# Optimization experiments

Measured on AMD Instinct MI355X. Metric: run time of the kernel, lower is better.

The kernel has to match this reference:

```python
import jax, jax.numpy as jnp
import numpy as np

VEC, HID, B, S = 1280, 128, 4, 256
EPS = 1e-5


def _ln(x):
    m = x.mean(-1, keepdims=True)
    v = ((x - m) ** 2).mean(-1, keepdims=True)
    return (x - m) / jnp.sqrt(v + EPS)


def _add_attn(q_in, kv_in, Wq, Wk, wv):
    # Additive (Bahdanau) attention: scores[b,i,j] = wv . tanh(q[b,i] + k[b,j])
    q = q_in @ Wq            # [B, Sq, H]
    k = kv_in @ Wk           # [B, Sk, H]
    feat = jnp.tanh(q[:, :, None, :] + k[:, None, :, :])   # [B, Sq, Sk, H]
    scores = jnp.einsum('bijh,h->bij', feat, wv)
    attn = jax.nn.softmax(scores, axis=-1)
    return jnp.einsum('bij,bjd->bid', attn, kv_in)          # values = kv_in


def _res_fc(x, W1, b1, W2, b2):
    return jnp.maximum(x @ W1 + b1, 0.0) @ W2 + b2 + x


def setup_inputs() -> dict:
    key = jax.random.key(0)
    ks = iter(jax.random.split(key, 64))
    d = {
        'X': jax.random.normal(next(ks), (B, S, VEC), dtype=jnp.float32),
        'lys_pos': 100,
    }
    sc = 0.02
    for i in (1, 2, 3, 4):
        d[f'Wq{i}'] = jax.random.normal(next(ks), (VEC, HID), dtype=jnp.float32) * sc
        d[f'Wk{i}'] = jax.random.normal(next(ks), (VEC, HID), dtype=jnp.float32) * sc
        d[f'wv{i}'] = jax.random.normal(next(ks), (HID,), dtype=jnp.float32) * sc
    for i in (1, 2, 3):
        d[f'rW1_{i}'] = jax.random.normal(next(ks), (VEC, HID), dtype=jnp.float32) * sc
        d[f'rb1_{i}'] = jnp.zeros((HID,), dtype=jnp.float32)
        d[f'rW2_{i}'] = jax.random.normal(next(ks), (HID, VEC), dtype=jnp.float32) * sc
        d[f'rb2_{i}'] = jnp.zeros((VEC,), dtype=jnp.float32)
    d['hW1'] = jax.random.normal(next(ks), (VEC, 32), dtype=jnp.float32) * sc
    d['hb1'] = jnp.zeros((32,), dtype=jnp.float32)
    d['hW2'] = jax.random.normal(next(ks), (32, 12), dtype=jnp.float32) * sc
    d['hb2'] = jnp.zeros((12,), dtype=jnp.float32)
    d['hW3'] = jax.random.normal(next(ks), (12, 2), dtype=jnp.float32) * sc
    d['hb3'] = jnp.zeros((2,), dtype=jnp.float32)
    return d


def reference(X, lys_pos,
              Wq1, Wk1, wv1, Wq2, Wk2, wv2, Wq3, Wk3, wv3, Wq4, Wk4, wv4,
              rW1_1, rb1_1, rW2_1, rb2_1,
              rW1_2, rb1_2, rW2_2, rb2_2,
              rW1_3, rb1_3, rW2_3, rb2_3,
              hW1, hb1, hW2, hb2, hW3, hb3):
    X = X.astype(jnp.float32)
    X = _ln(_add_attn(X, X, Wq1, Wk1, wv1) + X)
    X = _res_fc(X, rW1_1, rb1_1, rW2_1, rb2_1)
    X = _ln(_add_attn(X, X, Wq2, Wk2, wv2) + X)
    X = _res_fc(X, rW1_2, rb1_2, rW2_2, rb2_2)
    X = _ln(_add_attn(X, X, Wq3, Wk3, wv3) + X)
    X = _res_fc(X, rW1_3, rb1_3, rW2_3, rb2_3)
    X_lys = X[:, lys_pos, :][:, None, :]                    # [B, 1, VEC]
    X_lys = _ln(_add_attn(X_lys, X, Wq4, Wk4, wv4) + X_lys)
    h = jnp.maximum(X_lys @ hW1 + hb1, 0.0)                 # dropout = identity (eval)
    h = jnp.maximum(h @ hW2 + hb2, 0.0)
    logits = (h @ hW3 + hb3)[:, 0, :]                       # squeeze(1) -> [B, 2]
    return logits
```

## Files before the change

### kernel.cpp

```cpp
#include <hip/hip_runtime.h>


#define DEV __device__ __forceinline__

static constexpr int VEC = 1280;
static constexpr int HID = 128;
static constexpr int BB  = 4;
static constexpr int SS  = 256;
static constexpr int MROWS = BB * SS;

DEV float ftanh(float x) {
  float e = __expf(2.0f * x);
  return 1.0f - __fdividef(2.0f, e + 1.0f);
}

DEV float waveSum(float v) {
#pragma unroll
  for (int off = 32; off > 0; off >>= 1) v += __shfl_xor(v, off, 64);
  return v;
}
DEV float waveMax(float v) {
#pragma unroll
  for (int off = 32; off > 0; off >>= 1) v = fmaxf(v, __shfl_xor(v, off, 64));
  return v;
}
DEV float blockSum(float v, float* red) {
  v = waveSum(v);
  int tid = threadIdx.x;
  if ((tid & 63) == 0) red[tid >> 6] = v;
  __syncthreads();
  float r = (red[0] + red[1]) + (red[2] + red[3]);
  __syncthreads();
  return r;
}
DEV float blockMax(float v, float* red) {
  v = waveMax(v);
  int tid = threadIdx.x;
  if ((tid & 63) == 0) red[tid >> 6] = v;
  __syncthreads();
  float r = fmaxf(fmaxf(red[0], red[1]), fmaxf(red[2], red[3]));
  __syncthreads();
  return r;
}

template <int ZMODE, bool ABRELU, bool OBIAS, bool ORES>
__global__ __launch_bounds__(256) void gemm_k(
    const float* __restrict__ A, long sAb,
    const float* __restrict__ B0, const float* __restrict__ B1, int nSplitB,
    long sBb, int ldB,
    float* __restrict__ C, long sCb,
    const float* __restrict__ aBias, const float* __restrict__ oBias,
    const float* __restrict__ res,
    int N, int K, int kChunk) {
  const int n0 = blockIdx.x * 64;
  const int m0 = blockIdx.y * 64;
  const int z  = blockIdx.z;

  const float* Ab = A + (ZMODE == 0 ? (long)z * sAb : 0L);
  float*       Cb = C + (ZMODE == 0 ? (long)z * sCb : 0L);
  const float* Bsel;
  int nb;
  if (n0 < nSplitB) { Bsel = B0; nb = n0; } else { Bsel = B1; nb = n0 - nSplitB; }
  Bsel += (ZMODE == 0 ? (long)z * sBb : 0L);

  const int kBeg = (ZMODE == 1) ? z * kChunk : 0;
  const int kEnd = (ZMODE == 1) ? kBeg + kChunk : K;

  __shared__ float As[16][68];
  __shared__ float Bs[16][68];

  const int tid = threadIdx.x;
  const int tx = tid & 15, ty = tid >> 4;
  const int ar = tid >> 2, ac = (tid & 3) << 2;
  const int br = tid >> 4, bc = (tid & 15) << 2;

  float acc[4][4] = {};

  for (int kt = kBeg; kt < kEnd; kt += 16) {
    float4 a4 = *(const float4*)(Ab + (size_t)(m0 + ar) * K + kt + ac);
    float4 b4 = *(const float4*)(Bsel + (size_t)(kt + br) * ldB + nb + bc);
    if (ABRELU) {
      float4 bz = *(const float4*)(aBias + kt + ac);
      a4.x = fmaxf(a4.x + bz.x, 0.0f);
      a4.y = fmaxf(a4.y + bz.y, 0.0f);
      a4.z = fmaxf(a4.z + bz.z, 0.0f);
      a4.w = fmaxf(a4.w + bz.w, 0.0f);
    }
    __syncthreads();
    As[ac + 0][ar] = a4.x;
    As[ac + 1][ar] = a4.y;
    As[ac + 2][ar] = a4.z;
    As[ac + 3][ar] = a4.w;
    *(float4*)&Bs[br][bc] = b4;
    __syncthreads();
#pragma unroll
    for (int kk = 0; kk < 16; ++kk) {
      const float4 av = *(const float4*)&As[kk][ty << 2];
      const float4 bv = *(const float4*)&Bs[kk][tx << 2];
      const float a[4] = {av.x, av.y, av.z, av.w};
      const float b[4] = {bv.x, bv.y, bv.z, bv.w};
#pragma unroll
      for (int i = 0; i < 4; ++i)
#pragma unroll
        for (int j = 0; j < 4; ++j) acc[i][j] = fmaf(a[i], b[j], acc[i][j]);
    }
  }

#pragma unroll
  for (int i = 0; i < 4; ++i) {
    const int m = m0 + (ty << 2) + i;
#pragma unroll
    for (int j = 0; j < 4; ++j) {
      const int n = n0 + (tx << 2) + j;
      float v = acc[i][j];
      if (ZMODE == 1) {
        atomicAdd(&Cb[(size_t)m * N + n], v);
      } else {
        if (OBIAS) v += oBias[n];
        if (ORES) v += res[(size_t)m * N + n];
        Cb[(size_t)m * N + n] = v;
      }
    }
  }
}

__global__ __launch_bounds__(256) void scores_k(const float* __restrict__ QK,
                                                const float* __restrict__ wv,
                                                float* __restrict__ attn) {
  const int i = blockIdx.x, b = blockIdx.y;
  const int tid = threadIdx.x;
  __shared__ float qs[128], wvs[128];
  __shared__ float red[4];
  if (tid < 128) {
    qs[tid] = QK[((size_t)(b * 256 + i)) * 256 + tid];
    wvs[tid] = wv[tid];
  }
  __syncthreads();
  const float* Kr = QK + ((size_t)(b * 256 + tid)) * 256 + 128;
  float s = 0.0f;
#pragma unroll 8
  for (int h = 0; h < 128; h += 4) {
    float4 k4 = *(const float4*)(Kr + h);
    s += wvs[h + 0] * ftanh(qs[h + 0] + k4.x);
    s += wvs[h + 1] * ftanh(qs[h + 1] + k4.y);
    s += wvs[h + 2] * ftanh(qs[h + 2] + k4.z);
    s += wvs[h + 3] * ftanh(qs[h + 3] + k4.w);
  }
  const float mx = blockMax(s, red);
  const float e = __expf(s - mx);
  const float tot = blockSum(e, red);
  attn[((size_t)(b * 256 + i)) * 256 + tid] = e / tot;
}

__global__ __launch_bounds__(256) void ln_k(const float* __restrict__ A,
                                            const float* __restrict__ Xin,
                                            float* __restrict__ Y) {
  __shared__ float red[4];
  const int r = blockIdx.x, tid = threadIdx.x;
  const float* a = A + (size_t)r * VEC;
  const float* x = Xin + (size_t)r * VEC;
  float v[5];
  float sum = 0.0f;
#pragma unroll
  for (int k = 0; k < 5; ++k) {
    const int d = tid + k * 256;
    v[k] = a[d] + x[d];
    sum += v[k];
  }
  sum = blockSum(sum, red);
  const float m = sum * (1.0f / VEC);
  float sq = 0.0f;
#pragma unroll
  for (int k = 0; k < 5; ++k) {
    const float dl = v[k] - m;
    sq += dl * dl;
  }
  sq = blockSum(sq, red);
  const float rstd = rsqrtf(sq * (1.0f / VEC) + 1e-5f);
  float* y = Y + (size_t)r * VEC;
#pragma unroll
  for (int k = 0; k < 5; ++k) y[tid + k * 256] = (v[k] - m) * rstd;
}

__global__ __launch_bounds__(256) void scores4_k(const float* __restrict__ QK,
                                                 const float* __restrict__ wv,
                                                 const int* __restrict__ lys,
                                                 float* __restrict__ attn4) {
  const int b = blockIdx.x, tid = threadIdx.x;
  __shared__ float qs[128], wvs[128];
  __shared__ float red[4];
  const int lp = lys[0];
  if (tid < 128) {
    qs[tid] = QK[((size_t)(b * 256 + lp)) * 256 + tid];
    wvs[tid] = wv[tid];
  }
  __syncthreads();
  const float* Kr = QK + ((size_t)(b * 256 + tid)) * 256 + 128;
  float s = 0.0f;
#pragma unroll 8
  for (int h = 0; h < 128; h += 4) {
    float4 k4 = *(const float4*)(Kr + h);
    s += wvs[h + 0] * ftanh(qs[h + 0] + k4.x);
    s += wvs[h + 1] * ftanh(qs[h + 1] + k4.y);
    s += wvs[h + 2] * ftanh(qs[h + 2] + k4.z);
    s += wvs[h + 3] * ftanh(qs[h + 3] + k4.w);
  }
  const float mx = blockMax(s, red);
  const float e = __expf(s - mx);
  const float tot = blockSum(e, red);
  attn4[b * 256 + tid] = e / tot;
}

__global__ __launch_bounds__(256) void attn4_out_ln_k(const float* __restrict__ attn4,
                                                      const float* __restrict__ X3,
                                                      const int* __restrict__ lys,
                                                      float* __restrict__ Xlys) {
  const int b = blockIdx.x, tid = threadIdx.x;
  __shared__ float aw[256];
  __shared__ float red[4];
  aw[tid] = attn4[b * 256 + tid];
  __syncthreads();
  float acc[5] = {0, 0, 0, 0, 0};
  const float* Xb = X3 + (size_t)b * SS * VEC;
  for (int j = 0; j < 256; ++j) {
    const float a = aw[j];
    const float* xr = Xb + (size_t)j * VEC;
#pragma unroll
    for (int k = 0; k < 5; ++k) acc[k] = fmaf(a, xr[tid + k * 256], acc[k]);
  }
  const int lp = lys[0];
  const float* xq = Xb + (size_t)lp * VEC;
  float sum = 0.0f;
#pragma unroll
  for (int k = 0; k < 5; ++k) {
    acc[k] += xq[tid + k * 256];
    sum += acc[k];
  }
  sum = blockSum(sum, red);
  const float m = sum * (1.0f / VEC);
  float sq = 0.0f;
#pragma unroll
  for (int k = 0; k < 5; ++k) {
    const float dl = acc[k] - m;
    sq += dl * dl;
  }
  sq = blockSum(sq, red);
  const float rstd = rsqrtf(sq * (1.0f / VEC) + 1e-5f);
#pragma unroll
  for (int k = 0; k < 5; ++k) Xlys[b * VEC + tid + k * 256] = (acc[k] - m) * rstd;
}

__global__ __launch_bounds__(256) void head_k(const float* __restrict__ Xlys,
                                              const float* __restrict__ hW1,
                                              const float* __restrict__ hb1,
                                              const float* __restrict__ hW2,
                                              const float* __restrict__ hb2,
                                              const float* __restrict__ hW3,
                                              const float* __restrict__ hb3,
                                              float* __restrict__ out) {
  const int b = blockIdx.x, tid = threadIdx.x;
  __shared__ float xr[1280];
  __shared__ float partial[256];
  __shared__ float h1s[32], h2s[12];
  for (int k = tid; k < 1280; k += 256) xr[k] = Xlys[b * VEC + k];
  __syncthreads();
  const int n = tid & 31, s = tid >> 5;
  float p = 0.0f;
  for (int k = s * 160; k < s * 160 + 160; ++k) p = fmaf(xr[k], hW1[k * 32 + n], p);
  partial[tid] = p;
  __syncthreads();
  if (tid < 32) {
    float v = 0.0f;
#pragma unroll
    for (int s2 = 0; s2 < 8; ++s2) v += partial[s2 * 32 + tid];
    h1s[tid] = fmaxf(v + hb1[tid], 0.0f);
  }
  __syncthreads();
  if (tid < 12) {
    float v = 0.0f;
#pragma unroll
    for (int k = 0; k < 32; ++k) v = fmaf(h1s[k], hW2[k * 12 + tid], v);
    h2s[tid] = fmaxf(v + hb2[tid], 0.0f);
  }
  __syncthreads();
  if (tid < 2) {
    float v = 0.0f;
#pragma unroll
    for (int k = 0; k < 12; ++k) v = fmaf(h2s[k], hW3[k * 2 + tid], v);
    out[b * 2 + tid] = v + hb3[tid];
  }
}

extern "C" void kernel_launch(void* const* d_in, const int* in_sizes, int n_in,
                              void* d_out, int out_size, void* d_ws, size_t ws_size,
                              hipStream_t stream) {
  const float* X = (const float*)d_in[0];
  const int* lys = (const int*)d_in[1];
  const float* Wq[4] = {(const float*)d_in[2], (const float*)d_in[5],
                        (const float*)d_in[8], (const float*)d_in[11]};
  const float* Wk[4] = {(const float*)d_in[3], (const float*)d_in[6],
                        (const float*)d_in[9], (const float*)d_in[12]};
  const float* wv[4] = {(const float*)d_in[4], (const float*)d_in[7],
                        (const float*)d_in[10], (const float*)d_in[13]};
  const float* rW1[3] = {(const float*)d_in[14], (const float*)d_in[18],
                         (const float*)d_in[22]};
  const float* rb1[3] = {(const float*)d_in[15], (const float*)d_in[19],
                         (const float*)d_in[23]};
  const float* rW2[3] = {(const float*)d_in[16], (const float*)d_in[20],
                         (const float*)d_in[24]};
  const float* rb2[3] = {(const float*)d_in[17], (const float*)d_in[21],
                         (const float*)d_in[25]};
  const float* hW1 = (const float*)d_in[26];
  const float* hb1 = (const float*)d_in[27];
  const float* hW2 = (const float*)d_in[28];
  const float* hb2 = (const float*)d_in[29];
  const float* hW3 = (const float*)d_in[30];
  const float* hb3 = (const float*)d_in[31];
  float* out = (float*)d_out;

  float* ws = (float*)d_ws;
  float* QK    = ws;
  float* attn  = QK + 262144;
  float* big0  = attn + 262144;
  float* big1  = big0 + 1310720;
  float* big2  = big1 + 1310720;
  float* Hacc  = big2 + 1310720;
  float* attn4 = Hacc + 131072;
  float* Xlys  = attn4 + 1024;

  float* bufA[3] = {big0, big1, big0};
  float* bufY[3] = {big1, big2, big2};
  float* bufO[3] = {big0, big1, big0};

  const int NSPLIT_NONE = 1 << 30;
  const float* Xin = X;

  for (int l = 0; l < 3; ++l) {
    hipMemsetAsync(QK, 0, (size_t)MROWS * 256 * sizeof(float), stream);
    gemm_k<1, false, false, false><<<dim3(4, 16, 4), 256, 0, stream>>>(
        Xin, 0, Wq[l], Wk[l], HID, 0, HID, QK, 0, nullptr, nullptr, nullptr,
        256, VEC, 320);
    scores_k<<<dim3(SS, BB), 256, 0, stream>>>(QK, wv[l], attn);
    gemm_k<0, false, false, false><<<dim3(20, 4, 4), 256, 0, stream>>>(
        attn, (long)SS * SS, Xin, Xin, NSPLIT_NONE, (long)SS * VEC, VEC,
        bufA[l], (long)SS * VEC, nullptr, nullptr, nullptr, VEC, SS, 0);
    ln_k<<<dim3(MROWS), 256, 0, stream>>>(bufA[l], Xin, bufY[l]);
    hipMemsetAsync(Hacc, 0, (size_t)MROWS * HID * sizeof(float), stream);
    gemm_k<1, false, false, false><<<dim3(2, 16, 8), 256, 0, stream>>>(
        bufY[l], 0, rW1[l], rW1[l], NSPLIT_NONE, 0, HID, Hacc, 0, nullptr,
        nullptr, nullptr, HID, VEC, 160);
    gemm_k<0, true, true, true><<<dim3(20, 16, 1), 256, 0, stream>>>(
        Hacc, 0, rW2[l], rW2[l], NSPLIT_NONE, 0, VEC, bufO[l], 0, rb1[l],
        rb2[l], bufY[l], VEC, HID, 0);
    Xin = bufO[l];
  }

  hipMemsetAsync(QK, 0, (size_t)MROWS * 256 * sizeof(float), stream);
  gemm_k<1, false, false, false><<<dim3(4, 16, 4), 256, 0, stream>>>(
      Xin, 0, Wq[3], Wk[3], HID, 0, HID, QK, 0, nullptr, nullptr, nullptr,
      256, VEC, 320);
  scores4_k<<<dim3(BB), 256, 0, stream>>>(QK, wv[3], lys, attn4);
  attn4_out_ln_k<<<dim3(BB), 256, 0, stream>>>(attn4, Xin, lys, Xlys);
  head_k<<<dim3(BB), 256, 0, stream>>>(Xlys, hW1, hb1, hW2, hb2, hW3, hb3, out);
}
```

Measured before the change: 529.3 us.

## Replace atomic split-K with partial buffers, batch score rows, fuse tail kernels

Split-K GEMMs now write per-chunk partial buffers instead of doing atomicAdd into memset-zeroed outputs, and consumers sum the four partials on load. This removes the memsets and the atomics. The scores kernel handles 8 query rows per block so each K row load is reused across them. The residual add moves into the attention-output GEMM epilogue, leaving a simpler LN. The last layer computes only the K projection plus a single-row Q projection, and the four tail kernels are fused into one. Consumers now re-read four partials, which costs extra memory traffic.

```diff
diff --git a/kernel.cpp b/kernel.cpp
--- a/kernel.cpp
+++ b/kernel.cpp
@@ -43,9 +43,9 @@
   return r;
 }
 
-template <int ZMODE, bool ABRELU, bool OBIAS, bool ORES>
+template <int MODE, bool AFUSE, bool OBIAS, bool ORES>
 __global__ __launch_bounds__(256) void gemm_k(
-    const float* __restrict__ A, long sAb,
+    const float* __restrict__ A, long sAb, long aPart,
     const float* __restrict__ B0, const float* __restrict__ B1, int nSplitB,
     long sBb, int ldB,
     float* __restrict__ C, long sCb,
@@ -56,15 +56,16 @@
   const int m0 = blockIdx.y * 64;
   const int z  = blockIdx.z;
 
-  const float* Ab = A + (ZMODE == 0 ? (long)z * sAb : 0L);
-  float*       Cb = C + (ZMODE == 0 ? (long)z * sCb : 0L);
+  const float* Ab = A + (MODE == 0 ? (long)z * sAb : 0L);
+  float*       Cb = C + (long)z * sCb;
+  const float* resz = ORES ? (res + (MODE == 0 ? (long)z * sCb : 0L)) : nullptr;
   const float* Bsel;
   int nb;
   if (n0 < nSplitB) { Bsel = B0; nb = n0; } else { Bsel = B1; nb = n0 - nSplitB; }
-  Bsel += (ZMODE == 0 ? (long)z * sBb : 0L);
-
-  const int kBeg = (ZMODE == 1) ? z * kChunk : 0;
-  const int kEnd = (ZMODE == 1) ? kBeg + kChunk : K;
+  Bsel += (MODE == 0 ? (long)z * sBb : 0L);
+
+  const int kBeg = (MODE == 1) ? z * kChunk : 0;
+  const int kEnd = (MODE == 1) ? kBeg + kChunk : K;
 
   __shared__ float As[16][68];
   __shared__ float Bs[16][68];
@@ -77,15 +78,22 @@
   float acc[4][4] = {};
 
   for (int kt = kBeg; kt < kEnd; kt += 16) {
-    float4 a4 = *(const float4*)(Ab + (size_t)(m0 + ar) * K + kt + ac);
+    const size_t aoff = (size_t)(m0 + ar) * K + kt + ac;
+    float4 a4;
+    if (AFUSE) {
+      float4 p0 = *(const float4*)(Ab + aoff);
+      float4 p1 = *(const float4*)(Ab + aPart + aoff);
+      float4 p2 = *(const float4*)(Ab + 2 * aPart + aoff);
+      float4 p3 = *(const float4*)(Ab + 3 * aPart + aoff);
+      float4 bz = *(const float4*)(aBias + kt + ac);
+      a4.x = fmaxf(p0.x + p1.x + p2.x + p3.x + bz.x, 0.0f);
+      a4.y = fmaxf(p0.y + p1.y + p2.y + p3.y + bz.y, 0.0f);
+      a4.z = fmaxf(p0.z + p1.z + p2.z + p3.z + bz.z, 0.0f);
+      a4.w = fmaxf(p0.w + p1.w + p2.w + p3.w + bz.w, 0.0f);
+    } else {
+      a4 = *(const float4*)(Ab + aoff);
+    }
     float4 b4 = *(const float4*)(Bsel + (size_t)(kt + br) * ldB + nb + bc);
-    if (ABRELU) {
-      float4 bz = *(const float4*)(aBias + kt + ac);
-      a4.x = fmaxf(a4.x + bz.x, 0.0f);
-      a4.y = fmaxf(a4.y + bz.y, 0.0f);
-      a4.z = fmaxf(a4.z + bz.z, 0.0f);
-      a4.w = fmaxf(a4.w + bz.w, 0.0f);
-    }
     __syncthreads();
     As[ac + 0][ar] = a4.x;
     As[ac + 1][ar] = a4.y;
@@ -113,113 +121,137 @@
     for (int j = 0; j < 4; ++j) {
       const int n = n0 + (tx << 2) + j;
       float v = acc[i][j];
-      if (ZMODE == 1) {
-        atomicAdd(&Cb[(size_t)m * N + n], v);
-      } else {
-        if (OBIAS) v += oBias[n];
-        if (ORES) v += res[(size_t)m * N + n];
-        Cb[(size_t)m * N + n] = v;
-      }
+      if (OBIAS) v += oBias[n];
+      if (ORES) v += resz[(size_t)m * N + n];
+      Cb[(size_t)m * N + n] = v;
     }
   }
 }
 
-__global__ __launch_bounds__(256) void scores_k(const float* __restrict__ QK,
-                                                const float* __restrict__ wv,
-                                                float* __restrict__ attn) {
-  const int i = blockIdx.x, b = blockIdx.y;
+__global__ __launch_bounds__(256) void scores8_k(const float* __restrict__ QKp,
+                                                 long pStride,
+                                                 const float* __restrict__ wv,
+                                                 float* __restrict__ attn) {
+  const int b = blockIdx.y;
+  const int i0 = blockIdx.x * 8;
   const int tid = threadIdx.x;
+  __shared__ float qs[8][128];
+  __shared__ float wvs[128];
+  __shared__ float red[4];
+  for (int idx = tid; idx < 1024; idx += 256) {
+    const int r = idx >> 7, h = idx & 127;
+    const size_t off = ((size_t)(b * 256 + i0 + r)) * 256 + h;
+    qs[r][h] = QKp[off] + QKp[pStride + off] + QKp[2 * pStride + off] +
+               QKp[3 * pStride + off];
+  }
+  if (tid < 128) wvs[tid] = wv[tid];
+  __syncthreads();
+
+  const size_t kb = ((size_t)(b * 256 + tid)) * 256 + 128;
+  float s[8] = {0, 0, 0, 0, 0, 0, 0, 0};
+  for (int h = 0; h < 128; h += 4) {
+    float4 k0 = *(const float4*)(QKp + kb + h);
+    float4 k1 = *(const float4*)(QKp + pStride + kb + h);
+    float4 k2 = *(const float4*)(QKp + 2 * pStride + kb + h);
+    float4 k3 = *(const float4*)(QKp + 3 * pStride + kb + h);
+    const float kx = k0.x + k1.x + k2.x + k3.x;
+    const float ky = k0.y + k1.y + k2.y + k3.y;
+    const float kz = k0.z + k1.z + k2.z + k3.z;
+    const float kw = k0.w + k1.w + k2.w + k3.w;
+    const float w0 = wvs[h], w1 = wvs[h + 1], w2 = wvs[h + 2], w3 = wvs[h + 3];
+#pragma unroll
+    for (int r = 0; r < 8; ++r) {
+      s[r] += w0 * ftanh(qs[r][h] + kx) + w1 * ftanh(qs[r][h + 1] + ky) +
+              w2 * ftanh(qs[r][h + 2] + kz) + w3 * ftanh(qs[r][h + 3] + kw);
+    }
+  }
+#pragma unroll
+  for (int r = 0; r < 8; ++r) {
+    const float mx = blockMax(s[r], red);
+    const float e = __expf(s[r] - mx);
+    const float tot = blockSum(e, red);
+    attn[((size_t)(b * 256 + i0 + r)) * 256 + tid] = e / tot;
+  }
+}
+
+__global__ __launch_bounds__(256) void ln1_k(const float* __restrict__ A,
+                                             float* __restrict__ Y) {
+  __shared__ float red[4];
+  const int r = blockIdx.x, tid = threadIdx.x;
+  const float* a = A + (size_t)r * VEC;
+  float v[5];
+  float sum = 0.0f;
+#pragma unroll
+  for (int k = 0; k < 5; ++k) {
+    v[k] = a[tid + k * 256];
+    sum += v[k];
+  }
+  sum = blockSum(sum, red);
+  const float m = sum * (1.0f / VEC);
+  float sq = 0.0f;
+#pragma unroll
+  for (int k = 0; k < 5; ++k) {
+    const float dl = v[k] - m;
+    sq += dl * dl;
+  }
+  sq = blockSum(sq, red);
+  const float rstd = rsqrtf(sq * (1.0f / VEC) + 1e-5f);
+  float* y = Y + (size_t)r * VEC;
+#pragma unroll
+  for (int k = 0; k < 5; ++k) y[tid + k * 256] = (v[k] - m) * rstd;
+}
+
+__global__ __launch_bounds__(256) void tail4_k(
+    const float* __restrict__ K4p, long pStride,
+    const float* __restrict__ X3, const float* __restrict__ Wq4,
+    const float* __restrict__ wv4, const int* __restrict__ lys,
+    const float* __restrict__ hW1, const float* __restrict__ hb1,
+    const float* __restrict__ hW2, const float* __restrict__ hb2,
+    const float* __restrict__ hW3, const float* __restrict__ hb3,
+    float* __restrict__ out) {
+  const int b = blockIdx.x, tid = threadIdx.x;
+  __shared__ float xrow[1280];
   __shared__ float qs[128], wvs[128];
+  __shared__ float aw[256], partial[256];
   __shared__ float red[4];
-  if (tid < 128) {
-    qs[tid] = QK[((size_t)(b * 256 + i)) * 256 + tid];
-    wvs[tid] = wv[tid];
-  }
-  __syncthreads();
-  const float* Kr = QK + ((size_t)(b * 256 + tid)) * 256 + 128;
+  __shared__ float h1s[32], h2s[12];
+  const int lp = lys[0];
+
+  for (int k = tid; k < 1280; k += 256)
+    xrow[k] = X3[((size_t)(b * 256 + lp)) * VEC + k];
+  if (tid < 128) wvs[tid] = wv4[tid];
+  __syncthreads();
+
+  {
+    const int s = tid >> 7, h = tid & 127;
+    float acc = 0.0f;
+    const int k0 = s * 640;
+    for (int k = k0; k < k0 + 640; ++k)
+      acc = fmaf(xrow[k], Wq4[(size_t)k * HID + h], acc);
+    partial[tid] = acc;
+  }
+  __syncthreads();
+  if (tid < 128) qs[tid] = partial[tid] + partial[tid + 128];
+  __syncthreads();
+
+  const size_t kb = ((size_t)(b * 256 + tid)) * 128;
   float s = 0.0f;
-#pragma unroll 8
   for (int h = 0; h < 128; h += 4) {
-    float4 k4 = *(const float4*)(Kr + h);
-    s += wvs[h + 0] * ftanh(qs[h + 0] + k4.x);
-    s += wvs[h + 1] * ftanh(qs[h + 1] + k4.y);
-    s += wvs[h + 2] * ftanh(qs[h + 2] + k4.z);
-    s += wvs[h + 3] * ftanh(qs[h + 3] + k4.w);
+    float4 k0 = *(const float4*)(K4p + kb + h);
+    float4 k1 = *(const float4*)(K4p + pStride + kb + h);
+    float4 k2 = *(const float4*)(K4p + 2 * pStride + kb + h);
+    float4 k3 = *(const float4*)(K4p + 3 * pStride + kb + h);
+    s += wvs[h + 0] * ftanh(qs[h + 0] + k0.x + k1.x + k2.x + k3.x);
+    s += wvs[h + 1] * ftanh(qs[h + 1] + k0.y + k1.y + k2.y + k3.y);
+    s += wvs[h + 2] * ftanh(qs[h + 2] + k0.z + k1.z + k2.z + k3.z);
+    s += wvs[h + 3] * ftanh(qs[h + 3] + k0.w + k1.w + k2.w + k3.w);
   }
   const float mx = blockMax(s, red);
   const float e = __expf(s - mx);
   const float tot = blockSum(e, red);
-  attn[((size_t)(b * 256 + i)) * 256 + tid] = e / tot;
-}
-
-__global__ __launch_bounds__(256) void ln_k(const float* __restrict__ A,
-                                            const float* __restrict__ Xin,
-                                            float* __restrict__ Y) {
-  __shared__ float red[4];
-  const int r = blockIdx.x, tid = threadIdx.x;
-  const float* a = A + (size_t)r * VEC;
-  const float* x = Xin + (size_t)r * VEC;
-  float v[5];
-  float sum = 0.0f;
-#pragma unroll
-  for (int k = 0; k < 5; ++k) {
-    const int d = tid + k * 256;
-    v[k] = a[d] + x[d];
-    sum += v[k];
-  }
-  sum = blockSum(sum, red);
-  const float m = sum * (1.0f / VEC);
-  float sq = 0.0f;
-#pragma unroll
-  for (int k = 0; k < 5; ++k) {
-    const float dl = v[k] - m;
-    sq += dl * dl;
-  }
-  sq = blockSum(sq, red);
-  const float rstd = rsqrtf(sq * (1.0f / VEC) + 1e-5f);
-  float* y = Y + (size_t)r * VEC;
-#pragma unroll
-  for (int k = 0; k < 5; ++k) y[tid + k * 256] = (v[k] - m) * rstd;
-}
-
-__global__ __launch_bounds__(256) void scores4_k(const float* __restrict__ QK,
-                                                 const float* __restrict__ wv,
-                                                 const int* __restrict__ lys,
-                                                 float* __restrict__ attn4) {
-  const int b = blockIdx.x, tid = threadIdx.x;
-  __shared__ float qs[128], wvs[128];
-  __shared__ float red[4];
-  const int lp = lys[0];
-  if (tid < 128) {
-    qs[tid] = QK[((size_t)(b * 256 + lp)) * 256 + tid];
-    wvs[tid] = wv[tid];
-  }
-  __syncthreads();
-  const float* Kr = QK + ((size_t)(b * 256 + tid)) * 256 + 128;
-  float s = 0.0f;
-#pragma unroll 8
-  for (int h = 0; h < 128; h += 4) {
-    float4 k4 = *(const float4*)(Kr + h);
-    s += wvs[h + 0] * ftanh(qs[h + 0] + k4.x);
-    s += wvs[h + 1] * ftanh(qs[h + 1] + k4.y);
-    s += wvs[h + 2] * ftanh(qs[h + 2] + k4.z);
-    s += wvs[h + 3] * ftanh(qs[h + 3] + k4.w);
-  }
-  const float mx = blockMax(s, red);
-  const float e = __expf(s - mx);
-  const float tot = blockSum(e, red);
-  attn4[b * 256 + tid] = e / tot;
-}
-
-__global__ __launch_bounds__(256) void attn4_out_ln_k(const float* __restrict__ attn4,
-                                                      const float* __restrict__ X3,
-                                                      const int* __restrict__ lys,
-                                                      float* __restrict__ Xlys) {
-  const int b = blockIdx.x, tid = threadIdx.x;
-  __shared__ float aw[256];
-  __shared__ float red[4];
-  aw[tid] = attn4[b * 256 + tid];
-  __syncthreads();
+  aw[tid] = e / tot;
+  __syncthreads();
+
   float acc[5] = {0, 0, 0, 0, 0};
   const float* Xb = X3 + (size_t)b * SS * VEC;
   for (int j = 0; j < 256; ++j) {
@@ -228,12 +260,10 @@
 #pragma unroll
     for (int k = 0; k < 5; ++k) acc[k] = fmaf(a, xr[tid + k * 256], acc[k]);
   }
-  const int lp = lys[0];
-  const float* xq = Xb + (size_t)lp * VEC;
   float sum = 0.0f;
 #pragma unroll
   for (int k = 0; k < 5; ++k) {
-    acc[k] += xq[tid + k * 256];
+    acc[k] += xrow[tid + k * 256];
     sum += acc[k];
   }
   sum = blockSum(sum, red);
@@ -247,27 +277,16 @@
   sq = blockSum(sq, red);
   const float rstd = rsqrtf(sq * (1.0f / VEC) + 1e-5f);
 #pragma unroll
-  for (int k = 0; k < 5; ++k) Xlys[b * VEC + tid + k * 256] = (acc[k] - m) * rstd;
-}
-
-__global__ __launch_bounds__(256) void head_k(const float* __restrict__ Xlys,
-                                              const float* __restrict__ hW1,
-                                              const float* __restrict__ hb1,
-                                              const float* __restrict__ hW2,
-                                              const float* __restrict__ hb2,
-                                              const float* __restrict__ hW3,
-                                              const float* __restrict__ hb3,
-                                              float* __restrict__ out) {
-  const int b = blockIdx.x, tid = threadIdx.x;
-  __shared__ float xr[1280];
-  __shared__ float partial[256];
-  __shared__ float h1s[32], h2s[12];
-  for (int k = tid; k < 1280; k += 256) xr[k] = Xlys[b * VEC + k];
-  __syncthreads();
-  const int n = tid & 31, s = tid >> 5;
-  float p = 0.0f;
-  for (int k = s * 160; k < s * 160 + 160; ++k) p = fmaf(xr[k], hW1[k * 32 + n], p);
-  partial[tid] = p;
+  for (int k = 0; k < 5; ++k) xrow[tid + k * 256] = (acc[k] - m) * rstd;
+  __syncthreads();
+
+  {
+    const int n = tid & 31, sl = tid >> 5;
+    float p = 0.0f;
+    for (int k = sl * 160; k < sl * 160 + 160; ++k)
+      p = fmaf(xrow[k], hW1[(size_t)k * 32 + n], p);
+    partial[tid] = p;
+  }
   __syncthreads();
   if (tid < 32) {
     float v = 0.0f;
@@ -319,47 +338,42 @@
   float* out = (float*)d_out;
 
   float* ws = (float*)d_ws;
-  float* QK    = ws;
-  float* attn  = QK + 262144;
-  float* big0  = attn + 262144;
-  float* big1  = big0 + 1310720;
-  float* big2  = big1 + 1310720;
-  float* Hacc  = big2 + 1310720;
-  float* attn4 = Hacc + 131072;
-  float* Xlys  = attn4 + 1024;
-
-  float* bufA[3] = {big0, big1, big0};
-  float* bufY[3] = {big1, big2, big2};
-  float* bufO[3] = {big0, big1, big0};
-
+  float* QKp  = ws;
+  float* attn = QKp + 4 * 262144;
+  float* big0 = attn + 262144;
+  float* big1 = big0 + 1310720;
+  float* Yb   = big1 + 1310720;
+  float* Hp   = Yb + 1310720;
+
+  const long QK_PS = 262144;
+  const long H_PS  = 131072;
   const int NSPLIT_NONE = 1 << 30;
-  const float* Xin = X;
+
+  const float* P[3] = {X, big0, big1};
+  float* Q[3] = {big0, big1, big0};
 
   for (int l = 0; l < 3; ++l) {
-    hipMemsetAsync(QK, 0, (size_t)MROWS * 256 * sizeof(float), stream);
+    const float* Xin = P[l];
     gemm_k<1, false, false, false><<<dim3(4, 16, 4), 256, 0, stream>>>(
-        Xin, 0, Wq[l], Wk[l], HID, 0, HID, QK, 0, nullptr, nullptr, nullptr,
-        256, VEC, 320);
-    scores_k<<<dim3(SS, BB), 256, 0, stream>>>(QK, wv[l], attn);
-    gemm_k<0, false, false, false><<<dim3(20, 4, 4), 256, 0, stream>>>(
-        attn, (long)SS * SS, Xin, Xin, NSPLIT_NONE, (long)SS * VEC, VEC,
-        bufA[l], (long)SS * VEC, nullptr, nullptr, nullptr, VEC, SS, 0);
-    ln_k<<<dim3(MROWS), 256, 0, stream>>>(bufA[l], Xin, bufY[l]);
-    hipMemsetAsync(Hacc, 0, (size_t)MROWS * HID * sizeof(float), stream);
-    gemm_k<1, false, false, false><<<dim3(2, 16, 8), 256, 0, stream>>>(
-        bufY[l], 0, rW1[l], rW1[l], NSPLIT_NONE, 0, HID, Hacc, 0, nullptr,
-        nullptr, nullptr, HID, VEC, 160);
+        Xin, 0, 0, Wq[l], Wk[l], HID, 0, HID, QKp, QK_PS, nullptr, nullptr,
+        nullptr, 256, VEC, 320);
+    scores8_k<<<dim3(32, BB), 256, 0, stream>>>(QKp, QK_PS, wv[l], attn);
+    gemm_k<0, false, false, true><<<dim3(20, 4, 4), 256, 0, stream>>>(
+        attn, (long)SS * SS, 0, Xin, Xin, NSPLIT_NONE, (long)SS * VEC, VEC,
+        Q[l], (long)SS * VEC, nullptr, nullptr, Xin, VEC, SS, 0);
+    ln1_k<<<dim3(MROWS), 256, 0, stream>>>(Q[l], Yb);
+    gemm_k<1, false, false, false><<<dim3(2, 16, 4), 256, 0, stream>>>(
+        Yb, 0, 0, rW1[l], rW1[l], NSPLIT_NONE, 0, HID, Hp, H_PS, nullptr,
+        nullptr, nullptr, HID, VEC, 320);
     gemm_k<0, true, true, true><<<dim3(20, 16, 1), 256, 0, stream>>>(
-        Hacc, 0, rW2[l], rW2[l], NSPLIT_NONE, 0, VEC, bufO[l], 0, rb1[l],
-        rb2[l], bufY[l], VEC, HID, 0);
-    Xin = bufO[l];
-  }
-
-  hipMemsetAsync(QK, 0, (size_t)MROWS * 256 * sizeof(float), stream);
-  gemm_k<1, false, false, false><<<dim3(4, 16, 4), 256, 0, stream>>>(
-      Xin, 0, Wq[3], Wk[3], HID, 0, HID, QK, 0, nullptr, nullptr, nullptr,
-      256, VEC, 320);
-  scores4_k<<<dim3(BB), 256, 0, stream>>>(QK, wv[3], lys, attn4);
-  attn4_out_ln_k<<<dim3(BB), 256, 0, stream>>>(attn4, Xin, lys, Xlys);
-  head_k<<<dim3(BB), 256, 0, stream>>>(Xlys, hW1, hb1, hW2, hb2, hW3, hb3, out);
-}
+        Hp, 0, H_PS, rW2[l], rW2[l], NSPLIT_NONE, 0, VEC, Q[l], 0, rb1[l],
+        rb2[l], Yb, VEC, HID, 0);
+  }
+
+  const float* X3 = Q[2];
+  gemm_k<1, false, false, false><<<dim3(2, 16, 4), 256, 0, stream>>>(
+      X3, 0, 0, Wk[3], Wk[3], NSPLIT_NONE, 0, HID, QKp, H_PS, nullptr,
+      nullptr, nullptr, HID, VEC, 320);
+  tail4_k<<<dim3(BB), 256, 0, stream>>>(QKp, H_PS, X3, Wq[3], wv[3], lys,
+                                        hW1, hb1, hW2, hb2, hW3, hb3, out);
+}
```

Measured after the change: 605.6 us. 1.14x slower.
